# Performance work log

Hardware: AMD Instinct MI355X
Metric: run time of the kernel (lower is better)

Reference implementation:

```python
import jax, jax.numpy as jnp
import numpy as np

NUM_HEADS = 12
HEAD_DIM = 64
HIDDEN = NUM_HEADS * HEAD_DIM  # 768


def setup_inputs() -> dict:
    key = jax.random.key(0)
    ks = jax.random.split(key, 18)
    B, Ni, Nt, H = 8, 1024, 512, HIDDEN
    inp = {
        "hidden_states": jax.random.normal(ks[0], (B, Ni, H), jnp.float32),
        "text": jax.random.normal(ks[1], (B, Nt, H), jnp.float32),
    }
    names = ["Wq", "Wk", "Wv", "Wqt", "Wkt", "Wvt", "Wo"]
    for i, n in enumerate(names):
        inp[n] = jax.random.normal(ks[2 + i], (H, H), jnp.float32) * 0.02
        inp["b" + n[1:]] = jnp.zeros((H,), jnp.float32)
    return inp


def _split_heads(x):
    # [B, S, H] -> [B, h, S, dh]
    B, S, _ = x.shape
    return x.reshape(B, S, NUM_HEADS, HEAD_DIM).transpose(0, 2, 1, 3)


def _merge_heads(x):
    # [B, h, S, dh] -> [B, S, H]
    B, h, S, dh = x.shape
    return x.transpose(0, 2, 1, 3).reshape(B, S, h * dh)


def _attend(q, k, v):
    scale = 1.0 / jnp.sqrt(jnp.asarray(HEAD_DIM, q.dtype))
    scores = jnp.einsum("bhqd,bhkd->bhqk", q, k) * scale
    probs = jax.nn.softmax(scores, axis=-1)
    ctx = jnp.einsum("bhqk,bhkd->bhqd", probs, v)
    return ctx, probs


def reference(hidden_states, text, Wq, bq, Wk, bk, Wv, bv,
              Wqt, bqt, Wkt, bkt, Wvt, bvt, Wo, bo):
    q_i = _split_heads(hidden_states @ Wq + bq)
    k_i = _split_heads(hidden_states @ Wk + bk)
    v_i = _split_heads(hidden_states @ Wv + bv)
    q_t = _split_heads(text @ Wqt + bqt)
    k_t = _split_heads(text @ Wkt + bkt)
    v_t = _split_heads(text @ Wvt + bvt)

    ctx_ii, weights = _attend(q_i, k_i, v_i)   # img -> img (weights returned, vis=True)
    ctx_tt, _ = _attend(q_t, k_t, v_t)         # text -> text
    ctx_it, _ = _attend(q_i, k_t, v_t)         # img queries, text keys/values
    ctx_ti, _ = _attend(q_t, k_i, v_i)         # text queries, img keys/values

    out_img = (_merge_heads(ctx_ii) + _merge_heads(ctx_it)) * 0.5 @ Wo + bo
    out_text = (_merge_heads(ctx_tt) + _merge_heads(ctx_ti)) * 0.5 @ Wo + bo
    return out_img, out_text, weights
```

## Files before the change

kernel.cpp:

```cpp
#include <hip/hip_runtime.h>

typedef __attribute__((ext_vector_type(4))) float f32x4;
typedef __attribute__((ext_vector_type(8))) short short8;
typedef __attribute__((ext_vector_type(4))) unsigned short us4;
typedef unsigned short u16;
typedef unsigned char uchar;

__device__ __forceinline__ u16 f2b(float f) {
  union { float f; unsigned u; } a; a.f = f;
  unsigned r = a.u + 0x7fffu + ((a.u >> 16) & 1u);
  return (u16)(r >> 16);
}
#define SWZ(r, byteoff) ((((r) * 128) + (byteoff)) ^ (((r) & 7) << 4))

typedef __attribute__((address_space(1))) const void* gp1;
typedef __attribute__((address_space(3))) void* lp3;
__device__ __forceinline__ void gload16(const void* g, void* lds_wave_uniform_base) {
  __builtin_amdgcn_global_load_lds((gp1)g, (lp3)lds_wave_uniform_base, 16, 0, 0);
}

__global__ __launch_bounds__(256) void prep_kernel(
    const float* w0, const float* w1, const float* w2, const float* w3,
    const float* w4, const float* w5, const float* w6, u16* wt,
    const float* __restrict__ h, const float* __restrict__ tx, u16* __restrict__ xb)
{
  const int bid = blockIdx.x, t = threadIdx.x;
  if (bid < 1008) {
    __shared__ float tile[64][65];
    const float* Ws[7] = {w0, w1, w2, w3, w4, w5, w6};
    int z = bid / 144, rem = bid % 144;
    const float* W = Ws[z];
    u16* out = wt + (size_t)z * 589824;
    const int r0 = (rem / 12) * 64, c0 = (rem % 12) * 64;
#pragma unroll
    for (int i = 0; i < 4; ++i) {
      int idx = i * 256 + t;
      int r = idx >> 4, c = (idx & 15) * 4;
      f32x4 v = *(const f32x4*)(W + (size_t)(r0 + r) * 768 + (c0 + c));
      tile[r][c + 0] = v[0]; tile[r][c + 1] = v[1];
      tile[r][c + 2] = v[2]; tile[r][c + 3] = v[3];
    }
    __syncthreads();
#pragma unroll
    for (int i = 0; i < 4; ++i) {
      int idx = i * 256 + t;
      int rn = idx >> 4, c = (idx & 15) * 4;
      us4 o;
      o[0] = f2b(tile[c + 0][rn]); o[1] = f2b(tile[c + 1][rn]);
      o[2] = f2b(tile[c + 2][rn]); o[3] = f2b(tile[c + 3][rn]);
      *(us4*)(out + (size_t)(c0 + rn) * 768 + (r0 + c)) = o;
    }
  } else {
    size_t e = ((size_t)(bid - 1008) * 256 + t) * 8;
    const float* src; size_t off;
    if (e < 6291456) { src = h; off = e; } else { src = tx; off = e - 6291456; }
    f32x4 v0 = *(const f32x4*)(src + off), v1 = *(const f32x4*)(src + off + 4);
    short8 r;
    r[0] = (short)f2b(v0[0]); r[1] = (short)f2b(v0[1]); r[2] = (short)f2b(v0[2]); r[3] = (short)f2b(v0[3]);
    r[4] = (short)f2b(v1[0]); r[5] = (short)f2b(v1[1]); r[6] = (short)f2b(v1[2]); r[7] = (short)f2b(v1[3]);
    *(short8*)(xb + e) = r;
  }
}

__global__ __launch_bounds__(256) void proj_kernel(
    const u16* __restrict__ Xb, const u16* __restrict__ wt,
    const float* __restrict__ bq, const float* __restrict__ bk, const float* __restrict__ bv,
    const float* __restrict__ bqt, const float* __restrict__ bkt, const float* __restrict__ bvt,
    u16* __restrict__ qi, u16* __restrict__ ki, u16* __restrict__ vti,
    u16* __restrict__ qt, u16* __restrict__ ktx, u16* __restrict__ vtt)
{
  const int bid = blockIdx.x;
  const int wk = (bid & 7) * 216 + (bid >> 3);
  const bool img = wk < 1152;
  const int id = img ? wk : wk - 1152;
  const int y = img ? (id >> 6) : (id >> 5);
  const int x = img ? (id & 63) : (id & 31);
  const int z = y / 6, n0 = (y % 6) * 128, m0 = x * 128;
  const int S = img ? 1024 : 512, logS = img ? 10 : 9;
  const u16* X = img ? Xb : Xb + 6291456;
  const u16* Wt = wt + (img ? 0 : (size_t)3 * 589824) + (size_t)y * 98304;
  const float* bias = img ? (z == 0 ? bq : z == 1 ? bk : bv)
                          : (z == 0 ? bqt : z == 1 ? bkt : bvt);
  u16* out = img ? (z == 0 ? qi : z == 1 ? ki : vti)
                 : (z == 0 ? qt : z == 1 ? ktx : vtt);
  const bool vmode = (z == 2);
  __shared__ unsigned char sm[36864];
  unsigned char* Asm = sm;
  unsigned char* Bsm = sm + 16384;
  const int t = threadIdx.x, w = t >> 6, l = t & 63;
  const int wm = (w & 1) * 64, wn = (w >> 1) * 64;
  f32x4 acc[4][4] = {};
  for (int k0 = 0; k0 < 768; k0 += 64) {
#pragma unroll
    for (int j = 0; j < 4; ++j) {
      int chunk = j * 4 + w;
      int r = chunk * 8 + (l >> 3);
      int cb = ((l & 7) * 16) ^ ((r & 7) << 4);
      gload16(X + (size_t)(m0 + r) * 768 + k0 + cb / 2, Asm + chunk * 1024);
    }
#pragma unroll
    for (int j = 0; j < 4; ++j) {
      int chunk = j * 4 + w;
      int r = chunk * 8 + (l >> 3);
      int cb = ((l & 7) * 16) ^ ((r & 7) << 4);
      gload16(Wt + (size_t)r * 768 + k0 + cb / 2, Bsm + chunk * 1024);
    }
    __syncthreads();
#pragma unroll
    for (int kc = 0; kc < 2; ++kc) {
      short8 af[4], bfr[4];
      const int koff = (kc * 32 + (l >> 4) * 8) * 2;
#pragma unroll
      for (int ms = 0; ms < 4; ++ms) {
        int row = wm + ms * 16 + (l & 15);
        af[ms] = *(const short8*)(Asm + SWZ(row, koff));
      }
#pragma unroll
      for (int ns = 0; ns < 4; ++ns) {
        int row = wn + ns * 16 + (l & 15);
        bfr[ns] = *(const short8*)(Bsm + SWZ(row, koff));
      }
      __builtin_amdgcn_s_setprio(1);
#pragma unroll
      for (int ms = 0; ms < 4; ++ms)
#pragma unroll
        for (int ns = 0; ns < 4; ++ns)
          acc[ms][ns] = __builtin_amdgcn_mfma_f32_16x16x32_bf16(af[ms], bfr[ns], acc[ms][ns], 0, 0, 0);
      __builtin_amdgcn_s_setprio(0);
    }
    __syncthreads();
  }
  float bvv[4];
#pragma unroll
  for (int ns = 0; ns < 4; ++ns) bvv[ns] = bias[n0 + wn + ns * 16 + (l & 15)];
#pragma unroll
  for (int ms = 0; ms < 4; ++ms)
#pragma unroll
    for (int ns = 0; ns < 4; ++ns)
#pragma unroll
      for (int i = 0; i < 4; ++i) {
        u16 u = f2b(acc[ms][ns][i] + bvv[ns]);
        int mm = wm + ms * 16 + (l >> 4) * 4 + i;
        int nn = wn + ns * 16 + (l & 15);
        int row = vmode ? nn : mm, col = vmode ? mm : nn;
        *(u16*)(sm + row * 272 + col * 2) = u;
      }
  __syncthreads();
  if (!vmode) {
#pragma unroll
    for (int i = 0; i < 8; ++i) {
      int idx = i * 256 + t;
      int r = idx >> 4, c = (idx & 15) * 8;
      short8 v = *(const short8*)(sm + r * 272 + c * 2);
      int sg = m0 + r, b = sg >> logS, s = sg & (S - 1);
      int n = n0 + c, hh = n >> 6, d = n & 63;
      *(short8*)(out + (((size_t)b * 12 + hh) * S + s) * 64 + d) = v;
    }
  } else {
#pragma unroll
    for (int i = 0; i < 8; ++i) {
      int idx = i * 256 + t;
      int r = idx >> 4, c = (idx & 15) * 8;
      short8 v = *(const short8*)(sm + r * 272 + c * 2);
      int n = n0 + r, hh = n >> 6, d = n & 63;
      int sg = m0 + c, b = sg >> logS, s = sg & (S - 1);
      *(short8*)(out + (((size_t)b * 12 + hh) * 64 + d) * S + s) = v;
    }
  }
}

__device__ __forceinline__ void stage_k(const u16* Kp, int kt, uchar* Ksm, int w, int l) {
#pragma unroll
  for (int j = 0; j < 2; ++j) {
    int chunk = j * 4 + w;
    int r = chunk * 8 + (l >> 3);
    int cb = ((l & 7) * 16) ^ ((r & 7) << 4);
    gload16(Kp + (size_t)(kt * 64 + r) * 64 + cb / 2, Ksm + chunk * 1024);
  }
}
__device__ __forceinline__ void stage_v(const u16* Vp, int kt, int Sk, uchar* Vsm, int w, int l) {
#pragma unroll
  for (int j = 0; j < 2; ++j) {
    int chunk = j * 4 + w;
    int r = chunk * 8 + (l >> 3);
    int cb = ((l & 7) * 16) ^ ((r & 7) << 4);
    gload16(Vp + (size_t)r * Sk + kt * 64 + cb / 2, Vsm + chunk * 1024);
  }
}
__device__ __forceinline__ void qk8(const short8 qf[2], const uchar* Ksm, int l, f32x4 sfr[4]) {
  __builtin_amdgcn_s_setprio(1);
#pragma unroll
  for (int kc = 0; kc < 2; ++kc)
#pragma unroll
    for (int sub = 0; sub < 4; ++sub) {
      int row = sub * 16 + (l & 15);
      short8 kf = *(const short8*)(Ksm + SWZ(row, (kc * 32 + (l >> 4) * 8) * 2));
      sfr[sub] = __builtin_amdgcn_mfma_f32_16x16x32_bf16(qf[kc], kf, sfr[sub], 0, 0, 0);
    }
  __builtin_amdgcn_s_setprio(0);
}
__device__ __forceinline__ void pv8(const uchar* Pf, const uchar* Vsm, int l, f32x4 og[4]) {
  const uchar* base = Pf + (l & 15) * 272 + (l >> 4) * 32;
  f32x4 a0 = *(const f32x4*)(base);
  f32x4 a1 = *(const f32x4*)(base + 16);
  f32x4 b0 = *(const f32x4*)(base + 128);
  f32x4 b1 = *(const f32x4*)(base + 144);
  short8 pa0, pa1;
  pa0[0] = (short)f2b(a0[0]); pa0[1] = (short)f2b(a0[1]); pa0[2] = (short)f2b(a0[2]); pa0[3] = (short)f2b(a0[3]);
  pa0[4] = (short)f2b(a1[0]); pa0[5] = (short)f2b(a1[1]); pa0[6] = (short)f2b(a1[2]); pa0[7] = (short)f2b(a1[3]);
  pa1[0] = (short)f2b(b0[0]); pa1[1] = (short)f2b(b0[1]); pa1[2] = (short)f2b(b0[2]); pa1[3] = (short)f2b(b0[3]);
  pa1[4] = (short)f2b(b1[0]); pa1[5] = (short)f2b(b1[1]); pa1[6] = (short)f2b(b1[2]); pa1[7] = (short)f2b(b1[3]);
  __builtin_amdgcn_s_setprio(1);
#pragma unroll
  for (int ds = 0; ds < 4; ++ds) {
    int row = ds * 16 + (l & 15);
    short8 vb0 = *(const short8*)(Vsm + SWZ(row, ((l >> 4) * 8) * 2));
    short8 vb1 = *(const short8*)(Vsm + SWZ(row, (32 + (l >> 4) * 8) * 2));
    og[ds] = __builtin_amdgcn_mfma_f32_16x16x32_bf16(pa0, vb0, og[ds], 0, 0, 0);
    og[ds] = __builtin_amdgcn_mfma_f32_16x16x32_bf16(pa1, vb1, og[ds], 0, 0, 0);
  }
  __builtin_amdgcn_s_setprio(0);
}
__device__ __forceinline__ void red16(float v[4]) {
#pragma unroll
  for (int d = 1; d < 16; d <<= 1)
#pragma unroll
    for (int i = 0; i < 4; ++i) v[i] += __shfl_xor(v[i], d);
}
__device__ __forceinline__ void pass_unnorm(
    const u16* Kp, const u16* Vp, int Sk, const short8 qf[2],
    uchar* Ks0, uchar* Ks1, uchar* Vs0, uchar* Vs1, uchar* Pf,
    int w, int l, f32x4 og[4], float ll[4])
{
  const int nkt = Sk >> 6;
  stage_k(Kp, 0, Ks0, w, l);
  stage_v(Vp, 0, Sk, Vs0, w, l);
  __syncthreads();
  for (int kt = 0; kt < nkt; ++kt) {
    uchar* Kc = (kt & 1) ? Ks1 : Ks0;
    uchar* Vc = (kt & 1) ? Vs1 : Vs0;
    if (kt + 1 < nkt) {
      stage_k(Kp, kt + 1, (kt & 1) ? Ks0 : Ks1, w, l);
      stage_v(Vp, kt + 1, Sk, (kt & 1) ? Vs0 : Vs1, w, l);
    }
    f32x4 sfr[4] = {};
    qk8(qf, Kc, l, sfr);
#pragma unroll
    for (int sub = 0; sub < 4; ++sub)
#pragma unroll
      for (int i = 0; i < 4; ++i) {
        float p = __expf(sfr[sub][i] * 0.125f);
        ll[i] += p;
        *(float*)(Pf + ((l >> 4) * 4 + i) * 272 + (sub * 16 + (l & 15)) * 4) = p;
      }
    pv8(Pf, Vc, l, og);
    __syncthreads();
  }
}

__global__ __launch_bounds__(256) void attn_kernel(
    const u16* __restrict__ qi, const u16* __restrict__ ki, const u16* __restrict__ vti,
    const u16* __restrict__ qt, const u16* __restrict__ ktx, const u16* __restrict__ vtt,
    u16* __restrict__ cimg, u16* __restrict__ ctxt, float* __restrict__ weights)
{
  __shared__ uchar smem[50176];
  const int t = threadIdx.x, w = t >> 6, l = t & 63;
  uchar* Ks0 = smem;
  uchar* Ks1 = smem + 8192;
  uchar* Vs0 = smem + 16384;
  uchar* Vs1 = smem + 24576;
  uchar* Pf  = smem + 32768 + w * 4352;

  const int bid = blockIdx.x;
  const int wk = (bid & 7) * 288 + (bid >> 3);
  const bool img = wk < 1536;
  const int id = img ? wk : wk - 1536;
  const int x = img ? (id & 15) : (id & 7);
  const int head = img ? (id >> 4) : (id >> 3);
  const int b = head / 12, h = head % 12;
  const int Sq = img ? 1024 : 512;
  const int SkA = img ? 1024 : 512, SkB = img ? 512 : 1024;
  const u16* Qp = (img ? qi : qt) + (size_t)head * Sq * 64;
  const u16* KpA = (img ? ki : ktx) + (size_t)head * SkA * 64;
  const u16* VpA = (img ? vti : vtt) + (size_t)head * 64 * SkA;
  const u16* KpB = (img ? ktx : ki) + (size_t)head * SkB * 64;
  const u16* VpB = (img ? vtt : vti) + (size_t)head * 64 * SkB;
  u16* CTX = img ? cimg : ctxt;
  float* PROBS = img ? weights : nullptr;
  const int q0 = x * 64;

  short8 qf[2];
  {
    int row = q0 + w * 16 + (l & 15);
    qf[0] = *(const short8*)(Qp + (size_t)row * 64 + (l >> 4) * 8);
    qf[1] = *(const short8*)(Qp + (size_t)row * 64 + 32 + (l >> 4) * 8);
  }

  f32x4 of[4] = {};
  if (PROBS) {
    float ll[4] = {0.f, 0.f, 0.f, 0.f};
    const int nkt = SkA >> 6;
    stage_k(KpA, 0, Ks0, w, l);
    __syncthreads();
    for (int kt = 0; kt < nkt; ++kt) {
      uchar* Kc = (kt & 1) ? Ks1 : Ks0;
      if (kt + 1 < nkt) stage_k(KpA, kt + 1, (kt & 1) ? Ks0 : Ks1, w, l);
      f32x4 sfr[4] = {};
      qk8(qf, Kc, l, sfr);
#pragma unroll
      for (int sub = 0; sub < 4; ++sub)
#pragma unroll
        for (int i = 0; i < 4; ++i) ll[i] += __expf(sfr[sub][i] * 0.125f);
      __syncthreads();
    }
    stage_k(KpA, 0, Ks0, w, l);
    stage_v(VpA, 0, SkA, Vs0, w, l);
    red16(ll);
    float rl[4];
#pragma unroll
    for (int i = 0; i < 4; ++i) rl[i] = 1.0f / ll[i];
    __syncthreads();
    const size_t pbase = ((size_t)head * Sq + q0 + w * 16);
    for (int kt = 0; kt < nkt; ++kt) {
      uchar* Kc = (kt & 1) ? Ks1 : Ks0;
      uchar* Vc = (kt & 1) ? Vs1 : Vs0;
      if (kt + 1 < nkt) {
        stage_k(KpA, kt + 1, (kt & 1) ? Ks0 : Ks1, w, l);
        stage_v(VpA, kt + 1, SkA, (kt & 1) ? Vs0 : Vs1, w, l);
      }
      f32x4 sfr[4] = {};
      qk8(qf, Kc, l, sfr);
#pragma unroll
      for (int sub = 0; sub < 4; ++sub)
#pragma unroll
        for (int i = 0; i < 4; ++i) {
          float p = __expf(sfr[sub][i] * 0.125f) * rl[i];
          *(float*)(Pf + ((l >> 4) * 4 + i) * 272 + (sub * 16 + (l & 15)) * 4) = p;
        }
#pragma unroll
      for (int ps = 0; ps < 4; ++ps) {
        int row = ps * 4 + (l >> 4);
        f32x4 v = *(const f32x4*)(Pf + row * 272 + (l & 15) * 16);
        *(f32x4*)(PROBS + (pbase + row) * (size_t)SkA + kt * 64 + (l & 15) * 4) = v;
      }
      pv8(Pf, Vc, l, of);
      __syncthreads();
    }
#pragma unroll
    for (int ds = 0; ds < 4; ++ds) of[ds] *= 0.5f;
  } else {
    float ll[4] = {0.f, 0.f, 0.f, 0.f};
    pass_unnorm(KpA, VpA, SkA, qf, Ks0, Ks1, Vs0, Vs1, Pf, w, l, of, ll);
    red16(ll);
#pragma unroll
    for (int ds = 0; ds < 4; ++ds)
#pragma unroll
      for (int i = 0; i < 4; ++i) of[ds][i] *= 0.5f / ll[i];
  }
  {
    f32x4 og[4] = {};
    float l2[4] = {0.f, 0.f, 0.f, 0.f};
    pass_unnorm(KpB, VpB, SkB, qf, Ks0, Ks1, Vs0, Vs1, Pf, w, l, og, l2);
    red16(l2);
#pragma unroll
    for (int ds = 0; ds < 4; ++ds)
#pragma unroll
      for (int i = 0; i < 4; ++i) of[ds][i] += og[ds][i] * (0.5f / l2[i]);
  }
#pragma unroll
  for (int ds = 0; ds < 4; ++ds)
#pragma unroll
    for (int i = 0; i < 4; ++i)
      *(float*)(Pf + ((l >> 4) * 4 + i) * 272 + (ds * 16 + (l & 15)) * 4) = of[ds][i];
#pragma unroll
  for (int i = 0; i < 2; ++i) {
    int it = i * 64 + l;
    int r = it >> 3, cg = it & 7;
    f32x4 v0 = *(const f32x4*)(Pf + r * 272 + cg * 32);
    f32x4 v1 = *(const f32x4*)(Pf + r * 272 + cg * 32 + 16);
    short8 o;
    o[0] = (short)f2b(v0[0]); o[1] = (short)f2b(v0[1]); o[2] = (short)f2b(v0[2]); o[3] = (short)f2b(v0[3]);
    o[4] = (short)f2b(v1[0]); o[5] = (short)f2b(v1[1]); o[6] = (short)f2b(v1[2]); o[7] = (short)f2b(v1[3]);
    int s = q0 + w * 16 + r;
    *(short8*)(CTX + ((size_t)b * Sq + s) * 768 + h * 64 + cg * 8) = o;
  }
}

__global__ __launch_bounds__(256) void outproj_kernel(
    const u16* __restrict__ cimg, const u16* __restrict__ ctxt,
    const u16* __restrict__ Wto, const float* __restrict__ bias,
    float* __restrict__ out_img, float* __restrict__ out_text)
{
  const int bid = blockIdx.x;
  const int wk = (bid & 7) * 72 + (bid >> 3);
  const bool img = wk < 384;
  const int id = img ? wk : wk - 384;
  const int y = img ? (id >> 6) : (id >> 5);
  const int x = img ? (id & 63) : (id & 31);
  const u16* C = img ? cimg : ctxt;
  float* OUT = img ? out_img : out_text;
  const int m0 = x * 128, n0 = y * 128;
  __shared__ unsigned char sm[32768];
  unsigned char* Asm = sm;
  unsigned char* Bsm = sm + 16384;
  const int t = threadIdx.x, w = t >> 6, l = t & 63;
  const int wm = (w & 1) * 64, wn = (w >> 1) * 64;
  f32x4 acc[4][4] = {};
  for (int k0 = 0; k0 < 768; k0 += 64) {
#pragma unroll
    for (int j = 0; j < 4; ++j) {
      int chunk = j * 4 + w;
      int r = chunk * 8 + (l >> 3);
      int cb = ((l & 7) * 16) ^ ((r & 7) << 4);
      gload16(C + (size_t)(m0 + r) * 768 + k0 + cb / 2, Asm + chunk * 1024);
    }
#pragma unroll
    for (int j = 0; j < 4; ++j) {
      int chunk = j * 4 + w;
      int r = chunk * 8 + (l >> 3);
      int cb = ((l & 7) * 16) ^ ((r & 7) << 4);
      gload16(Wto + (size_t)(n0 + r) * 768 + k0 + cb / 2, Bsm + chunk * 1024);
    }
    __syncthreads();
#pragma unroll
    for (int kc = 0; kc < 2; ++kc) {
      short8 af[4], bfr[4];
      const int koff = (kc * 32 + (l >> 4) * 8) * 2;
#pragma unroll
      for (int ms = 0; ms < 4; ++ms) {
        int row = wm + ms * 16 + (l & 15);
        af[ms] = *(const short8*)(Asm + SWZ(row, koff));
      }
#pragma unroll
      for (int ns = 0; ns < 4; ++ns) {
        int row = wn + ns * 16 + (l & 15);
        bfr[ns] = *(const short8*)(Bsm + SWZ(row, koff));
      }
      __builtin_amdgcn_s_setprio(1);
#pragma unroll
      for (int ms = 0; ms < 4; ++ms)
#pragma unroll
        for (int ns = 0; ns < 4; ++ns)
          acc[ms][ns] = __builtin_amdgcn_mfma_f32_16x16x32_bf16(af[ms], bfr[ns], acc[ms][ns], 0, 0, 0);
      __builtin_amdgcn_s_setprio(0);
    }
    __syncthreads();
  }
#pragma unroll
  for (int ms = 0; ms < 4; ++ms)
#pragma unroll
    for (int ns = 0; ns < 4; ++ns) {
      float bv = bias[n0 + wn + ns * 16 + (l & 15)];
#pragma unroll
      for (int i = 0; i < 4; ++i) {
        int mm = m0 + wm + ms * 16 + (l >> 4) * 4 + i;
        int nn = n0 + wn + ns * 16 + (l & 15);
        OUT[(size_t)mm * 768 + nn] = acc[ms][ns][i] + bv;
      }
    }
}

extern "C" void kernel_launch(void* const* d_in, const int* in_sizes, int n_in,
                              void* d_out, int out_size, void* d_ws, size_t ws_size,
                              hipStream_t stream)
{
  const float* hidden = (const float*)d_in[0];
  const float* text   = (const float*)d_in[1];
  const float* Wq  = (const float*)d_in[2];  const float* bq  = (const float*)d_in[3];
  const float* Wk  = (const float*)d_in[4];  const float* bk  = (const float*)d_in[5];
  const float* Wv  = (const float*)d_in[6];  const float* bv  = (const float*)d_in[7];
  const float* Wqt = (const float*)d_in[8];  const float* bqt = (const float*)d_in[9];
  const float* Wkt = (const float*)d_in[10]; const float* bkt = (const float*)d_in[11];
  const float* Wvt = (const float*)d_in[12]; const float* bvt = (const float*)d_in[13];
  const float* Wo  = (const float*)d_in[14]; const float* bo  = (const float*)d_in[15];

  u16* wt   = (u16*)d_ws;
  u16* xb   = wt + 7 * 589824;
  u16* qi   = xb + 9437184;
  u16* ki   = qi + 6291456;
  u16* vti  = ki + 6291456;
  u16* qt   = vti + 6291456;
  u16* ktx  = qt + 3145728;
  u16* vtt  = ktx + 3145728;
  u16* cimg = vtt + 3145728;
  u16* ctxt = cimg + 6291456;

  float* out_img  = (float*)d_out;
  float* out_text = out_img + 6291456;
  float* weights  = out_text + 3145728;

  prep_kernel<<<5616, 256, 0, stream>>>(Wq, Wk, Wv, Wqt, Wkt, Wvt, Wo, wt,
                                        hidden, text, xb);
  proj_kernel<<<1728, 256, 0, stream>>>(xb, wt, bq, bk, bv, bqt, bkt, bvt,
                                        qi, ki, vti, qt, ktx, vtt);
  attn_kernel<<<2304, 256, 0, stream>>>(qi, ki, vti, qt, ktx, vtt,
                                        cimg, ctxt, weights);
  outproj_kernel<<<576, 256, 0, stream>>>(cimg, ctxt, wt + 6 * 589824, bo,
                                          out_img, out_text);
}
```

Before: 319.7 us.

## Load K/V fragments directly from global and use packed bf16 conversion

The attention kernel stops staging K and V tiles through double-buffered shared memory with block-wide barriers. Each wave now reads its MFMA operand fragments straight from global memory (relying on L1/L2), and shared memory shrinks to the per-wave probability scratch. Separately, the manual round-to-nearest bf16 conversion is replaced with the packed v_cvt_pk_bf16_f32 instruction. Dropping the barriers and LDS traffic lets waves run independently and may raise occupancy. The cost is that the four waves in a block no longer share K/V loads, so global and cache traffic rises and load latency is less hidden.

```diff
diff --git a/kernel.cpp b/kernel.cpp
--- a/kernel.cpp
+++ b/kernel.cpp
@@ -10,6 +10,17 @@
   union { float f; unsigned u; } a; a.f = f;
   unsigned r = a.u + 0x7fffu + ((a.u >> 16) & 1u);
   return (u16)(r >> 16);
+}
+__device__ __forceinline__ unsigned cvtpk2(float lo, float hi) {
+  unsigned r;
+  asm("v_cvt_pk_bf16_f32 %0, %1, %2" : "=v"(r) : "v"(lo), "v"(hi));
+  return r;
+}
+__device__ __forceinline__ short8 cvt8(f32x4 a, f32x4 b) {
+  union { unsigned u[4]; short8 s; } r;
+  r.u[0] = cvtpk2(a[0], a[1]); r.u[1] = cvtpk2(a[2], a[3]);
+  r.u[2] = cvtpk2(b[0], b[1]); r.u[3] = cvtpk2(b[2], b[3]);
+  return r.s;
 }
 #define SWZ(r, byteoff) ((((r) * 128) + (byteoff)) ^ (((r) & 7) << 4))
 
@@ -45,20 +56,17 @@
     for (int i = 0; i < 4; ++i) {
       int idx = i * 256 + t;
       int rn = idx >> 4, c = (idx & 15) * 4;
-      us4 o;
-      o[0] = f2b(tile[c + 0][rn]); o[1] = f2b(tile[c + 1][rn]);
-      o[2] = f2b(tile[c + 2][rn]); o[3] = f2b(tile[c + 3][rn]);
-      *(us4*)(out + (size_t)(c0 + rn) * 768 + (r0 + c)) = o;
+      union { us4 o; unsigned u[2]; } o;
+      o.u[0] = cvtpk2(tile[c + 0][rn], tile[c + 1][rn]);
+      o.u[1] = cvtpk2(tile[c + 2][rn], tile[c + 3][rn]);
+      *(us4*)(out + (size_t)(c0 + rn) * 768 + (r0 + c)) = o.o;
     }
   } else {
     size_t e = ((size_t)(bid - 1008) * 256 + t) * 8;
     const float* src; size_t off;
     if (e < 6291456) { src = h; off = e; } else { src = tx; off = e - 6291456; }
     f32x4 v0 = *(const f32x4*)(src + off), v1 = *(const f32x4*)(src + off + 4);
-    short8 r;
-    r[0] = (short)f2b(v0[0]); r[1] = (short)f2b(v0[1]); r[2] = (short)f2b(v0[2]); r[3] = (short)f2b(v0[3]);
-    r[4] = (short)f2b(v1[0]); r[5] = (short)f2b(v1[1]); r[6] = (short)f2b(v1[2]); r[7] = (short)f2b(v1[3]);
-    *(short8*)(xb + e) = r;
+    *(short8*)(xb + e) = cvt8(v0, v1);
   }
 }
 
@@ -169,55 +177,42 @@
   }
 }
 
-__device__ __forceinline__ void stage_k(const u16* Kp, int kt, uchar* Ksm, int w, int l) {
-#pragma unroll
-  for (int j = 0; j < 2; ++j) {
-    int chunk = j * 4 + w;
-    int r = chunk * 8 + (l >> 3);
-    int cb = ((l & 7) * 16) ^ ((r & 7) << 4);
-    gload16(Kp + (size_t)(kt * 64 + r) * 64 + cb / 2, Ksm + chunk * 1024);
-  }
-}
-__device__ __forceinline__ void stage_v(const u16* Vp, int kt, int Sk, uchar* Vsm, int w, int l) {
-#pragma unroll
-  for (int j = 0; j < 2; ++j) {
-    int chunk = j * 4 + w;
-    int r = chunk * 8 + (l >> 3);
-    int cb = ((l & 7) * 16) ^ ((r & 7) << 4);
-    gload16(Vp + (size_t)r * Sk + kt * 64 + cb / 2, Vsm + chunk * 1024);
-  }
-}
-__device__ __forceinline__ void qk8(const short8 qf[2], const uchar* Ksm, int l, f32x4 sfr[4]) {
+__device__ __forceinline__ void qk_direct(const short8 qf[2], const u16* __restrict__ Kt,
+                                          int l, f32x4 sfr[4]) {
+  short8 kf[8];
+#pragma unroll
+  for (int kc = 0; kc < 2; ++kc)
+#pragma unroll
+    for (int sub = 0; sub < 4; ++sub)
+      kf[kc * 4 + sub] = *(const short8*)(Kt + (size_t)(sub * 16 + (l & 15)) * 64 + kc * 32 + (l >> 4) * 8);
   __builtin_amdgcn_s_setprio(1);
 #pragma unroll
   for (int kc = 0; kc < 2; ++kc)
 #pragma unroll
-    for (int sub = 0; sub < 4; ++sub) {
-      int row = sub * 16 + (l & 15);
-      short8 kf = *(const short8*)(Ksm + SWZ(row, (kc * 32 + (l >> 4) * 8) * 2));
-      sfr[sub] = __builtin_amdgcn_mfma_f32_16x16x32_bf16(qf[kc], kf, sfr[sub], 0, 0, 0);
-    }
+    for (int sub = 0; sub < 4; ++sub)
+      sfr[sub] = __builtin_amdgcn_mfma_f32_16x16x32_bf16(qf[kc], kf[kc * 4 + sub], sfr[sub], 0, 0, 0);
   __builtin_amdgcn_s_setprio(0);
 }
-__device__ __forceinline__ void pv8(const uchar* Pf, const uchar* Vsm, int l, f32x4 og[4]) {
+__device__ __forceinline__ void pv_direct(const uchar* Pf, const u16* __restrict__ Vt,
+                                          int Sk, int l, f32x4 og[4]) {
   const uchar* base = Pf + (l & 15) * 272 + (l >> 4) * 32;
   f32x4 a0 = *(const f32x4*)(base);
   f32x4 a1 = *(const f32x4*)(base + 16);
   f32x4 b0 = *(const f32x4*)(base + 128);
   f32x4 b1 = *(const f32x4*)(base + 144);
-  short8 pa0, pa1;
-  pa0[0] = (short)f2b(a0[0]); pa0[1] = (short)f2b(a0[1]); pa0[2] = (short)f2b(a0[2]); pa0[3] = (short)f2b(a0[3]);
-  pa0[4] = (short)f2b(a1[0]); pa0[5] = (short)f2b(a1[1]); pa0[6] = (short)f2b(a1[2]); pa0[7] = (short)f2b(a1[3]);
-  pa1[0] = (short)f2b(b0[0]); pa1[1] = (short)f2b(b0[1]); pa1[2] = (short)f2b(b0[2]); pa1[3] = (short)f2b(b0[3]);
-  pa1[4] = (short)f2b(b1[0]); pa1[5] = (short)f2b(b1[1]); pa1[6] = (short)f2b(b1[2]); pa1[7] = (short)f2b(b1[3]);
+  short8 pa0 = cvt8(a0, a1), pa1 = cvt8(b0, b1);
+  short8 vb[8];
+#pragma unroll
+  for (int ds = 0; ds < 4; ++ds) {
+    const u16* vr = Vt + (size_t)(ds * 16 + (l & 15)) * Sk + (l >> 4) * 8;
+    vb[ds * 2]     = *(const short8*)(vr);
+    vb[ds * 2 + 1] = *(const short8*)(vr + 32);
+  }
   __builtin_amdgcn_s_setprio(1);
 #pragma unroll
   for (int ds = 0; ds < 4; ++ds) {
-    int row = ds * 16 + (l & 15);
-    short8 vb0 = *(const short8*)(Vsm + SWZ(row, ((l >> 4) * 8) * 2));
-    short8 vb1 = *(const short8*)(Vsm + SWZ(row, (32 + (l >> 4) * 8) * 2));
-    og[ds] = __builtin_amdgcn_mfma_f32_16x16x32_bf16(pa0, vb0, og[ds], 0, 0, 0);
-    og[ds] = __builtin_amdgcn_mfma_f32_16x16x32_bf16(pa1, vb1, og[ds], 0, 0, 0);
+    og[ds] = __builtin_amdgcn_mfma_f32_16x16x32_bf16(pa0, vb[ds * 2], og[ds], 0, 0, 0);
+    og[ds] = __builtin_amdgcn_mfma_f32_16x16x32_bf16(pa1, vb[ds * 2 + 1], og[ds], 0, 0, 0);
   }
   __builtin_amdgcn_s_setprio(0);
 }
@@ -228,23 +223,13 @@
     for (int i = 0; i < 4; ++i) v[i] += __shfl_xor(v[i], d);
 }
 __device__ __forceinline__ void pass_unnorm(
-    const u16* Kp, const u16* Vp, int Sk, const short8 qf[2],
-    uchar* Ks0, uchar* Ks1, uchar* Vs0, uchar* Vs1, uchar* Pf,
-    int w, int l, f32x4 og[4], float ll[4])
+    const u16* __restrict__ Kp, const u16* __restrict__ Vp, int Sk,
+    const short8 qf[2], uchar* Pf, int l, f32x4 og[4], float ll[4])
 {
   const int nkt = Sk >> 6;
-  stage_k(Kp, 0, Ks0, w, l);
-  stage_v(Vp, 0, Sk, Vs0, w, l);
-  __syncthreads();
   for (int kt = 0; kt < nkt; ++kt) {
-    uchar* Kc = (kt & 1) ? Ks1 : Ks0;
-    uchar* Vc = (kt & 1) ? Vs1 : Vs0;
-    if (kt + 1 < nkt) {
-      stage_k(Kp, kt + 1, (kt & 1) ? Ks0 : Ks1, w, l);
-      stage_v(Vp, kt + 1, Sk, (kt & 1) ? Vs0 : Vs1, w, l);
-    }
     f32x4 sfr[4] = {};
-    qk8(qf, Kc, l, sfr);
+    qk_direct(qf, Kp + (size_t)kt * 4096, l, sfr);
 #pragma unroll
     for (int sub = 0; sub < 4; ++sub)
 #pragma unroll
@@ -253,8 +238,7 @@
         ll[i] += p;
         *(float*)(Pf + ((l >> 4) * 4 + i) * 272 + (sub * 16 + (l & 15)) * 4) = p;
       }
-    pv8(Pf, Vc, l, og);
-    __syncthreads();
+    pv_direct(Pf, Vp + kt * 64, Sk, l, og);
   }
 }
 
@@ -263,13 +247,9 @@
     const u16* __restrict__ qt, const u16* __restrict__ ktx, const u16* __restrict__ vtt,
     u16* __restrict__ cimg, u16* __restrict__ ctxt, float* __restrict__ weights)
 {
-  __shared__ uchar smem[50176];
+  __shared__ uchar Pf_all[17408];
   const int t = threadIdx.x, w = t >> 6, l = t & 63;
-  uchar* Ks0 = smem;
-  uchar* Ks1 = smem + 8192;
-  uchar* Vs0 = smem + 16384;
-  uchar* Vs1 = smem + 24576;
-  uchar* Pf  = smem + 32768 + w * 4352;
+  uchar* Pf = Pf_all + w * 4352;
 
   const int bid = blockIdx.x;
   const int wk = (bid & 7) * 288 + (bid >> 3);
@@ -300,36 +280,22 @@
   if (PROBS) {
     float ll[4] = {0.f, 0.f, 0.f, 0.f};
     const int nkt = SkA >> 6;
-    stage_k(KpA, 0, Ks0, w, l);
-    __syncthreads();
     for (int kt = 0; kt < nkt; ++kt) {
-      uchar* Kc = (kt & 1) ? Ks1 : Ks0;
-      if (kt + 1 < nkt) stage_k(KpA, kt + 1, (kt & 1) ? Ks0 : Ks1, w, l);
       f32x4 sfr[4] = {};
-      qk8(qf, Kc, l, sfr);
+      qk_direct(qf, KpA + (size_t)kt * 4096, l, sfr);
 #pragma unroll
       for (int sub = 0; sub < 4; ++sub)
 #pragma unroll
         for (int i = 0; i < 4; ++i) ll[i] += __expf(sfr[sub][i] * 0.125f);
-      __syncthreads();
-    }
-    stage_k(KpA, 0, Ks0, w, l);
-    stage_v(VpA, 0, SkA, Vs0, w, l);
+    }
     red16(ll);
     float rl[4];
 #pragma unroll
     for (int i = 0; i < 4; ++i) rl[i] = 1.0f / ll[i];
-    __syncthreads();
     const size_t pbase = ((size_t)head * Sq + q0 + w * 16);
     for (int kt = 0; kt < nkt; ++kt) {
-      uchar* Kc = (kt & 1) ? Ks1 : Ks0;
-      uchar* Vc = (kt & 1) ? Vs1 : Vs0;
-      if (kt + 1 < nkt) {
-        stage_k(KpA, kt + 1, (kt & 1) ? Ks0 : Ks1, w, l);
-        stage_v(VpA, kt + 1, SkA, (kt & 1) ? Vs0 : Vs1, w, l);
-      }
       f32x4 sfr[4] = {};
-      qk8(qf, Kc, l, sfr);
+      qk_direct(qf, KpA + (size_t)kt * 4096, l, sfr);
 #pragma unroll
       for (int sub = 0; sub < 4; ++sub)
 #pragma unroll
@@ -343,14 +309,13 @@
         f32x4 v = *(const f32x4*)(Pf + row * 272 + (l & 15) * 16);
         *(f32x4*)(PROBS + (pbase + row) * (size_t)SkA + kt * 64 + (l & 15) * 4) = v;
       }
-      pv8(Pf, Vc, l, of);
-      __syncthreads();
+      pv_direct(Pf, VpA + kt * 64, SkA, l, of);
     }
 #pragma unroll
     for (int ds = 0; ds < 4; ++ds) of[ds] *= 0.5f;
   } else {
     float ll[4] = {0.f, 0.f, 0.f, 0.f};
-    pass_unnorm(KpA, VpA, SkA, qf, Ks0, Ks1, Vs0, Vs1, Pf, w, l, of, ll);
+    pass_unnorm(KpA, VpA, SkA, qf, Pf, l, of, ll);
     red16(ll);
 #pragma unroll
     for (int ds = 0; ds < 4; ++ds)
@@ -360,7 +325,7 @@
   {
     f32x4 og[4] = {};
     float l2[4] = {0.f, 0.f, 0.f, 0.f};
-    pass_unnorm(KpB, VpB, SkB, qf, Ks0, Ks1, Vs0, Vs1, Pf, w, l, og, l2);
+    pass_unnorm(KpB, VpB, SkB, qf, Pf, l, og, l2);
     red16(l2);
 #pragma unroll
     for (int ds = 0; ds < 4; ++ds)
@@ -378,11 +343,8 @@
     int r = it >> 3, cg = it & 7;
     f32x4 v0 = *(const f32x4*)(Pf + r * 272 + cg * 32);
     f32x4 v1 = *(const f32x4*)(Pf + r * 272 + cg * 32 + 16);
-    short8 o;
-    o[0] = (short)f2b(v0[0]); o[1] = (short)f2b(v0[1]); o[2] = (short)f2b(v0[2]); o[3] = (short)f2b(v0[3]);
-    o[4] = (short)f2b(v1[0]); o[5] = (short)f2b(v1[1]); o[6] = (short)f2b(v1[2]); o[7] = (short)f2b(v1[3]);
     int s = q0 + w * 16 + r;
-    *(short8*)(CTX + ((size_t)b * Sq + s) * 768 + h * 64 + cg * 8) = o;
+    *(short8*)(CTX + ((size_t)b * Sq + s) * 768 + h * 64 + cg * 8) = cvt8(v0, v1);
   }
 }
 
```

New measurement: 661.3 us. +106.8%, slower.

## Process two query tiles per attention block and use packed bf16 conversion

Applied to the files above, without the earlier changes.

Each attention block now handles 128 query rows (two 64-row sub-tiles per wave) instead of 64. K and V fragments are loaded from LDS once into registers and reused for both sub-tiles, halving the grid and the K/V global/LDS staging traffic per query. Scalar float-to-bf16 rounding is replaced by the hardware packed v_cvt_pk_bf16_f32 instruction. The trade is higher register pressure, which may lower occupancy, and fewer blocks to fill the GPU.

```diff
diff --git a/kernel.cpp b/kernel.cpp
--- a/kernel.cpp
+++ b/kernel.cpp
@@ -10,6 +10,17 @@
   union { float f; unsigned u; } a; a.f = f;
   unsigned r = a.u + 0x7fffu + ((a.u >> 16) & 1u);
   return (u16)(r >> 16);
+}
+__device__ __forceinline__ unsigned cvtpk2(float lo, float hi) {
+  unsigned r;
+  asm("v_cvt_pk_bf16_f32 %0, %1, %2" : "=v"(r) : "v"(lo), "v"(hi));
+  return r;
+}
+__device__ __forceinline__ short8 cvt8(f32x4 a, f32x4 b) {
+  union { unsigned u[4]; short8 s; } r;
+  r.u[0] = cvtpk2(a[0], a[1]); r.u[1] = cvtpk2(a[2], a[3]);
+  r.u[2] = cvtpk2(b[0], b[1]); r.u[3] = cvtpk2(b[2], b[3]);
+  return r.s;
 }
 #define SWZ(r, byteoff) ((((r) * 128) + (byteoff)) ^ (((r) & 7) << 4))
 
@@ -45,20 +56,17 @@
     for (int i = 0; i < 4; ++i) {
       int idx = i * 256 + t;
       int rn = idx >> 4, c = (idx & 15) * 4;
-      us4 o;
-      o[0] = f2b(tile[c + 0][rn]); o[1] = f2b(tile[c + 1][rn]);
-      o[2] = f2b(tile[c + 2][rn]); o[3] = f2b(tile[c + 3][rn]);
-      *(us4*)(out + (size_t)(c0 + rn) * 768 + (r0 + c)) = o;
+      union { us4 o; unsigned u[2]; } o;
+      o.u[0] = cvtpk2(tile[c + 0][rn], tile[c + 1][rn]);
+      o.u[1] = cvtpk2(tile[c + 2][rn], tile[c + 3][rn]);
+      *(us4*)(out + (size_t)(c0 + rn) * 768 + (r0 + c)) = o.o;
     }
   } else {
     size_t e = ((size_t)(bid - 1008) * 256 + t) * 8;
     const float* src; size_t off;
     if (e < 6291456) { src = h; off = e; } else { src = tx; off = e - 6291456; }
     f32x4 v0 = *(const f32x4*)(src + off), v1 = *(const f32x4*)(src + off + 4);
-    short8 r;
-    r[0] = (short)f2b(v0[0]); r[1] = (short)f2b(v0[1]); r[2] = (short)f2b(v0[2]); r[3] = (short)f2b(v0[3]);
-    r[4] = (short)f2b(v1[0]); r[5] = (short)f2b(v1[1]); r[6] = (short)f2b(v1[2]); r[7] = (short)f2b(v1[3]);
-    *(short8*)(xb + e) = r;
+    *(short8*)(xb + e) = cvt8(v0, v1);
   }
 }
 
@@ -187,50 +195,61 @@
     gload16(Vp + (size_t)r * Sk + kt * 64 + cb / 2, Vsm + chunk * 1024);
   }
 }
-__device__ __forceinline__ void qk8(const short8 qf[2], const uchar* Ksm, int l, f32x4 sfr[4]) {
-  __builtin_amdgcn_s_setprio(1);
+__device__ __forceinline__ void kfrags(const uchar* Ksm, int l, short8 kf[8]) {
 #pragma unroll
   for (int kc = 0; kc < 2; ++kc)
 #pragma unroll
     for (int sub = 0; sub < 4; ++sub) {
       int row = sub * 16 + (l & 15);
-      short8 kf = *(const short8*)(Ksm + SWZ(row, (kc * 32 + (l >> 4) * 8) * 2));
-      sfr[sub] = __builtin_amdgcn_mfma_f32_16x16x32_bf16(qf[kc], kf, sfr[sub], 0, 0, 0);
-    }
+      kf[kc * 4 + sub] = *(const short8*)(Ksm + SWZ(row, (kc * 32 + (l >> 4) * 8) * 2));
+    }
+}
+__device__ __forceinline__ void vfrags(const uchar* Vsm, int l, short8 vb[8]) {
+#pragma unroll
+  for (int ds = 0; ds < 4; ++ds) {
+    int row = ds * 16 + (l & 15);
+    vb[ds * 2]     = *(const short8*)(Vsm + SWZ(row, ((l >> 4) * 8) * 2));
+    vb[ds * 2 + 1] = *(const short8*)(Vsm + SWZ(row, (32 + (l >> 4) * 8) * 2));
+  }
+}
+__device__ __forceinline__ void qk_mfma2(const short8 qf[2][2], const short8 kf[8], f32x4 sfr[2][4]) {
+  __builtin_amdgcn_s_setprio(1);
+#pragma unroll
+  for (int m = 0; m < 2; ++m)
+#pragma unroll
+    for (int kc = 0; kc < 2; ++kc)
+#pragma unroll
+      for (int sub = 0; sub < 4; ++sub)
+        sfr[m][sub] = __builtin_amdgcn_mfma_f32_16x16x32_bf16(qf[m][kc], kf[kc * 4 + sub], sfr[m][sub], 0, 0, 0);
   __builtin_amdgcn_s_setprio(0);
 }
-__device__ __forceinline__ void pv8(const uchar* Pf, const uchar* Vsm, int l, f32x4 og[4]) {
+__device__ __forceinline__ void pv8v(const uchar* Pf, const short8 vb[8], int l, f32x4 og[4]) {
   const uchar* base = Pf + (l & 15) * 272 + (l >> 4) * 32;
   f32x4 a0 = *(const f32x4*)(base);
   f32x4 a1 = *(const f32x4*)(base + 16);
   f32x4 b0 = *(const f32x4*)(base + 128);
   f32x4 b1 = *(const f32x4*)(base + 144);
-  short8 pa0, pa1;
-  pa0[0] = (short)f2b(a0[0]); pa0[1] = (short)f2b(a0[1]); pa0[2] = (short)f2b(a0[2]); pa0[3] = (short)f2b(a0[3]);
-  pa0[4] = (short)f2b(a1[0]); pa0[5] = (short)f2b(a1[1]); pa0[6] = (short)f2b(a1[2]); pa0[7] = (short)f2b(a1[3]);
-  pa1[0] = (short)f2b(b0[0]); pa1[1] = (short)f2b(b0[1]); pa1[2] = (short)f2b(b0[2]); pa1[3] = (short)f2b(b0[3]);
-  pa1[4] = (short)f2b(b1[0]); pa1[5] = (short)f2b(b1[1]); pa1[6] = (short)f2b(b1[2]); pa1[7] = (short)f2b(b1[3]);
+  short8 pa0 = cvt8(a0, a1), pa1 = cvt8(b0, b1);
   __builtin_amdgcn_s_setprio(1);
 #pragma unroll
   for (int ds = 0; ds < 4; ++ds) {
-    int row = ds * 16 + (l & 15);
-    short8 vb0 = *(const short8*)(Vsm + SWZ(row, ((l >> 4) * 8) * 2));
-    short8 vb1 = *(const short8*)(Vsm + SWZ(row, (32 + (l >> 4) * 8) * 2));
-    og[ds] = __builtin_amdgcn_mfma_f32_16x16x32_bf16(pa0, vb0, og[ds], 0, 0, 0);
-    og[ds] = __builtin_amdgcn_mfma_f32_16x16x32_bf16(pa1, vb1, og[ds], 0, 0, 0);
+    og[ds] = __builtin_amdgcn_mfma_f32_16x16x32_bf16(pa0, vb[ds * 2], og[ds], 0, 0, 0);
+    og[ds] = __builtin_amdgcn_mfma_f32_16x16x32_bf16(pa1, vb[ds * 2 + 1], og[ds], 0, 0, 0);
   }
   __builtin_amdgcn_s_setprio(0);
 }
-__device__ __forceinline__ void red16(float v[4]) {
+__device__ __forceinline__ void red16_2(float v[2][4]) {
 #pragma unroll
   for (int d = 1; d < 16; d <<= 1)
 #pragma unroll
-    for (int i = 0; i < 4; ++i) v[i] += __shfl_xor(v[i], d);
+    for (int m = 0; m < 2; ++m)
+#pragma unroll
+      for (int i = 0; i < 4; ++i) v[m][i] += __shfl_xor(v[m][i], d);
 }
 __device__ __forceinline__ void pass_unnorm(
-    const u16* Kp, const u16* Vp, int Sk, const short8 qf[2],
-    uchar* Ks0, uchar* Ks1, uchar* Vs0, uchar* Vs1, uchar* Pf,
-    int w, int l, f32x4 og[4], float ll[4])
+    const u16* __restrict__ Kp, const u16* __restrict__ Vp, int Sk,
+    const short8 qf[2][2], uchar* Ks0, uchar* Ks1, uchar* Vs0, uchar* Vs1, uchar* Pf,
+    int w, int l, f32x4 og[2][4], float ll[2][4])
 {
   const int nkt = Sk >> 6;
   stage_k(Kp, 0, Ks0, w, l);
@@ -243,17 +262,24 @@
       stage_k(Kp, kt + 1, (kt & 1) ? Ks0 : Ks1, w, l);
       stage_v(Vp, kt + 1, Sk, (kt & 1) ? Vs0 : Vs1, w, l);
     }
-    f32x4 sfr[4] = {};
-    qk8(qf, Kc, l, sfr);
-#pragma unroll
-    for (int sub = 0; sub < 4; ++sub)
-#pragma unroll
-      for (int i = 0; i < 4; ++i) {
-        float p = __expf(sfr[sub][i] * 0.125f);
-        ll[i] += p;
-        *(float*)(Pf + ((l >> 4) * 4 + i) * 272 + (sub * 16 + (l & 15)) * 4) = p;
-      }
-    pv8(Pf, Vc, l, og);
+    short8 kf[8];
+    kfrags(Kc, l, kf);
+    f32x4 sfr[2][4] = {};
+    qk_mfma2(qf, kf, sfr);
+    short8 vb[8];
+    vfrags(Vc, l, vb);
+#pragma unroll
+    for (int m = 0; m < 2; ++m) {
+#pragma unroll
+      for (int sub = 0; sub < 4; ++sub)
+#pragma unroll
+        for (int i = 0; i < 4; ++i) {
+          float p = __expf(sfr[m][sub][i] * 0.125f);
+          ll[m][i] += p;
+          *(float*)(Pf + ((l >> 4) * 4 + i) * 272 + (sub * 16 + (l & 15)) * 4) = p;
+        }
+      pv8v(Pf, vb, l, og[m]);
+    }
     __syncthreads();
   }
 }
@@ -272,11 +298,11 @@
   uchar* Pf  = smem + 32768 + w * 4352;
 
   const int bid = blockIdx.x;
-  const int wk = (bid & 7) * 288 + (bid >> 3);
-  const bool img = wk < 1536;
-  const int id = img ? wk : wk - 1536;
-  const int x = img ? (id & 15) : (id & 7);
-  const int head = img ? (id >> 4) : (id >> 3);
+  const int wk = (bid & 7) * 144 + (bid >> 3);
+  const bool img = wk < 768;
+  const int id = img ? wk : wk - 768;
+  const int x = img ? (id & 7) : (id & 3);
+  const int head = img ? (id >> 3) : (id >> 2);
   const int b = head / 12, h = head % 12;
   const int Sq = img ? 1024 : 512;
   const int SkA = img ? 1024 : 512, SkB = img ? 512 : 1024;
@@ -287,40 +313,46 @@
   const u16* VpB = (img ? vtt : vti) + (size_t)head * 64 * SkB;
   u16* CTX = img ? cimg : ctxt;
   float* PROBS = img ? weights : nullptr;
-  const int q0 = x * 64;
-
-  short8 qf[2];
-  {
-    int row = q0 + w * 16 + (l & 15);
-    qf[0] = *(const short8*)(Qp + (size_t)row * 64 + (l >> 4) * 8);
-    qf[1] = *(const short8*)(Qp + (size_t)row * 64 + 32 + (l >> 4) * 8);
-  }
-
-  f32x4 of[4] = {};
+  const int q0 = x * 128;
+
+  short8 qf[2][2];
+#pragma unroll
+  for (int m = 0; m < 2; ++m) {
+    int row = q0 + m * 64 + w * 16 + (l & 15);
+    qf[m][0] = *(const short8*)(Qp + (size_t)row * 64 + (l >> 4) * 8);
+    qf[m][1] = *(const short8*)(Qp + (size_t)row * 64 + 32 + (l >> 4) * 8);
+  }
+
+  f32x4 of[2][4] = {};
   if (PROBS) {
-    float ll[4] = {0.f, 0.f, 0.f, 0.f};
+    float ll[2][4] = {};
     const int nkt = SkA >> 6;
     stage_k(KpA, 0, Ks0, w, l);
     __syncthreads();
     for (int kt = 0; kt < nkt; ++kt) {
       uchar* Kc = (kt & 1) ? Ks1 : Ks0;
       if (kt + 1 < nkt) stage_k(KpA, kt + 1, (kt & 1) ? Ks0 : Ks1, w, l);
-      f32x4 sfr[4] = {};
-      qk8(qf, Kc, l, sfr);
-#pragma unroll
-      for (int sub = 0; sub < 4; ++sub)
-#pragma unroll
-        for (int i = 0; i < 4; ++i) ll[i] += __expf(sfr[sub][i] * 0.125f);
+      short8 kf[8];
+      kfrags(Kc, l, kf);
+      f32x4 sfr[2][4] = {};
+      qk_mfma2(qf, kf, sfr);
+#pragma unroll
+      for (int m = 0; m < 2; ++m)
+#pragma unroll
+        for (int sub = 0; sub < 4; ++sub)
+#pragma unroll
+          for (int i = 0; i < 4; ++i) ll[m][i] += __expf(sfr[m][sub][i] * 0.125f);
       __syncthreads();
     }
     stage_k(KpA, 0, Ks0, w, l);
     stage_v(VpA, 0, SkA, Vs0, w, l);
-    red16(ll);
-    float rl[4];
-#pragma unroll
-    for (int i = 0; i < 4; ++i) rl[i] = 1.0f / ll[i];
-    __syncthreads();
-    const size_t pbase = ((size_t)head * Sq + q0 + w * 16);
+    red16_2(ll);
+    float rl[2][4];
+#pragma unroll
+    for (int m = 0; m < 2; ++m)
+#pragma unroll
+      for (int i = 0; i < 4; ++i) rl[m][i] = 1.0f / ll[m][i];
+    __syncthreads();
     for (int kt = 0; kt < nkt; ++kt) {
       uchar* Kc = (kt & 1) ? Ks1 : Ks0;
       uchar* Vc = (kt & 1) ? Vs1 : Vs0;
@@ -328,61 +360,75 @@
         stage_k(KpA, kt + 1, (kt & 1) ? Ks0 : Ks1, w, l);
         stage_v(VpA, kt + 1, SkA, (kt & 1) ? Vs0 : Vs1, w, l);
       }
-      f32x4 sfr[4] = {};
-      qk8(qf, Kc, l, sfr);
-#pragma unroll
-      for (int sub = 0; sub < 4; ++sub)
-#pragma unroll
-        for (int i = 0; i < 4; ++i) {
-          float p = __expf(sfr[sub][i] * 0.125f) * rl[i];
-          *(float*)(Pf + ((l >> 4) * 4 + i) * 272 + (sub * 16 + (l & 15)) * 4) = p;
+      short8 kf[8];
+      kfrags(Kc, l, kf);
+      f32x4 sfr[2][4] = {};
+      qk_mfma2(qf, kf, sfr);
+      short8 vb[8];
+      vfrags(Vc, l, vb);
+#pragma unroll
+      for (int m = 0; m < 2; ++m) {
+#pragma unroll
+        for (int sub = 0; sub < 4; ++sub)
+#pragma unroll
+          for (int i = 0; i < 4; ++i) {
+            float p = __expf(sfr[m][sub][i] * 0.125f) * rl[m][i];
+            *(float*)(Pf + ((l >> 4) * 4 + i) * 272 + (sub * 16 + (l & 15)) * 4) = p;
+          }
+        const size_t pbase = ((size_t)head * Sq + q0 + m * 64 + w * 16);
+#pragma unroll
+        for (int ps = 0; ps < 4; ++ps) {
+          int row = ps * 4 + (l >> 4);
+          f32x4 v = *(const f32x4*)(Pf + row * 272 + (l & 15) * 16);
+          *(f32x4*)(PROBS + (pbase + row) * (size_t)SkA + kt * 64 + (l & 15) * 4) = v;
         }
-#pragma unroll
-      for (int ps = 0; ps < 4; ++ps) {
-        int row = ps * 4 + (l >> 4);
-        f32x4 v = *(const f32x4*)(Pf + row * 272 + (l & 15) * 16);
-        *(f32x4*)(PROBS + (pbase + row) * (size_t)SkA + kt * 64 + (l & 15) * 4) = v;
-      }
-      pv8(Pf, Vc, l, of);
+        pv8v(Pf, vb, l, of[m]);
+      }
       __syncthreads();
     }
 #pragma unroll
-    for (int ds = 0; ds < 4; ++ds) of[ds] *= 0.5f;
+    for (int m = 0; m < 2; ++m)
+#pragma unroll
+      for (int ds = 0; ds < 4; ++ds) of[m][ds] *= 0.5f;
   } else {
-    float ll[4] = {0.f, 0.f, 0.f, 0.f};
+    float ll[2][4] = {};
     pass_unnorm(KpA, VpA, SkA, qf, Ks0, Ks1, Vs0, Vs1, Pf, w, l, of, ll);
-    red16(ll);
+    red16_2(ll);
+#pragma unroll
+    for (int m = 0; m < 2; ++m)
+#pragma unroll
+      for (int ds = 0; ds < 4; ++ds)
+#pragma unroll
+        for (int i = 0; i < 4; ++i) of[m][ds][i] *= 0.5f / ll[m][i];
+  }
+  {
+    f32x4 og[2][4] = {};
+    float l2[2][4] = {};
+    pass_unnorm(KpB, VpB, SkB, qf, Ks0, Ks1, Vs0, Vs1, Pf, w, l, og, l2);
+    red16_2(l2);
+#pragma unroll
+    for (int m = 0; m < 2; ++m)
+#pragma unroll
+      for (int ds = 0; ds < 4; ++ds)
+#pragma unroll
+        for (int i = 0; i < 4; ++i) of[m][ds][i] += og[m][ds][i] * (0.5f / l2[m][i]);
+  }
+#pragma unroll
+  for (int m = 0; m < 2; ++m) {
 #pragma unroll
     for (int ds = 0; ds < 4; ++ds)
 #pragma unroll
-      for (int i = 0; i < 4; ++i) of[ds][i] *= 0.5f / ll[i];
-  }
-  {
-    f32x4 og[4] = {};
-    float l2[4] = {0.f, 0.f, 0.f, 0.f};
-    pass_unnorm(KpB, VpB, SkB, qf, Ks0, Ks1, Vs0, Vs1, Pf, w, l, og, l2);
-    red16(l2);
-#pragma unroll
-    for (int ds = 0; ds < 4; ++ds)
-#pragma unroll
-      for (int i = 0; i < 4; ++i) of[ds][i] += og[ds][i] * (0.5f / l2[i]);
-  }
-#pragma unroll
-  for (int ds = 0; ds < 4; ++ds)
-#pragma unroll
-    for (int i = 0; i < 4; ++i)
-      *(float*)(Pf + ((l >> 4) * 4 + i) * 272 + (ds * 16 + (l & 15)) * 4) = of[ds][i];
-#pragma unroll
-  for (int i = 0; i < 2; ++i) {
-    int it = i * 64 + l;
-    int r = it >> 3, cg = it & 7;
-    f32x4 v0 = *(const f32x4*)(Pf + r * 272 + cg * 32);
-    f32x4 v1 = *(const f32x4*)(Pf + r * 272 + cg * 32 + 16);
-    short8 o;
-    o[0] = (short)f2b(v0[0]); o[1] = (short)f2b(v0[1]); o[2] = (short)f2b(v0[2]); o[3] = (short)f2b(v0[3]);
-    o[4] = (short)f2b(v1[0]); o[5] = (short)f2b(v1[1]); o[6] = (short)f2b(v1[2]); o[7] = (short)f2b(v1[3]);
-    int s = q0 + w * 16 + r;
-    *(short8*)(CTX + ((size_t)b * Sq + s) * 768 + h * 64 + cg * 8) = o;
+      for (int i = 0; i < 4; ++i)
+        *(float*)(Pf + ((l >> 4) * 4 + i) * 272 + (ds * 16 + (l & 15)) * 4) = of[m][ds][i];
+#pragma unroll
+    for (int i = 0; i < 2; ++i) {
+      int it = i * 64 + l;
+      int r = it >> 3, cg = it & 7;
+      f32x4 v0 = *(const f32x4*)(Pf + r * 272 + cg * 32);
+      f32x4 v1 = *(const f32x4*)(Pf + r * 272 + cg * 32 + 16);
+      int s = q0 + m * 64 + w * 16 + r;
+      *(short8*)(CTX + ((size_t)b * Sq + s) * 768 + h * 64 + cg * 8) = cvt8(v0, v1);
+    }
   }
 }
 
@@ -493,7 +539,7 @@
                                         hidden, text, xb);
   proj_kernel<<<1728, 256, 0, stream>>>(xb, wt, bq, bk, bv, bqt, bkt, bvt,
                                         qi, ki, vti, qt, ktx, vtt);
-  attn_kernel<<<2304, 256, 0, stream>>>(qi, ki, vti, qt, ktx, vtt,
+  attn_kernel<<<1152, 256, 0, stream>>>(qi, ki, vti, qt, ktx, vtt,
                                         cimg, ctxt, weights);
   outproj_kernel<<<576, 256, 0, stream>>>(cimg, ctxt, wt + 6 * 589824, bo,
                                           out_img, out_text);
```

New measurement: 327.7 us. 1.02x slower.
